# Kernel optimization log

Hardware: AMD Instinct MI355X
Metric: run time of the kernel (lower is better)

The kernel has to match this reference:

```python
import jax, jax.numpy as jnp
import numpy as np

B, N, D, E = 8, 10000, 64, 160000


def setup_inputs() -> dict:
    key = jax.random.key(0)
    ks = jax.random.split(key, 7)
    x = jax.random.normal(ks[0], (B, N, D), dtype=jnp.float32)
    W0 = jax.random.normal(ks[1], (D, D), dtype=jnp.float32) / np.sqrt(D)
    W1 = jax.random.normal(ks[2], (D, D), dtype=jnp.float32) / np.sqrt(D)
    W2 = jax.random.normal(ks[3], (D, D), dtype=jnp.float32) / np.sqrt(D)
    adj_vals = jax.random.uniform(ks[4], (E,), dtype=jnp.float32)
    adj_rows = jax.random.randint(ks[5], (E,), 0, N, dtype=jnp.int32)
    adj_cols = jax.random.randint(ks[6], (E,), 0, N, dtype=jnp.int32)
    return {"x": x, "W0": W0, "W1": W1, "W2": W2,
            "adj_vals": adj_vals, "adj_rows": adj_rows, "adj_cols": adj_cols}


def _spmm(vals, rows, cols, h):
    # h: [B, N, D]; shared sparse adj in COO. out[b, r] += vals[e] * h[b, c]
    msg = h[:, cols, :] * vals[None, :, None]          # [B, E, D]
    return jnp.zeros_like(h).at[:, rows, :].add(msg)   # scatter-add over rows


def _layer(h, W, vals, rows, cols):
    h = jax.nn.relu(jnp.einsum('bnd,df->bnf', h, W))   # Linear (no bias) + act
    return _spmm(vals, rows, cols, h)                  # adj @ h per sample


def reference(x, W0, W1, W2, adj_vals, adj_rows, adj_cols):
    out = _layer(x, W0.T, adj_vals, adj_rows, adj_cols)
    out = _layer(out, W1.T, adj_vals, adj_rows, adj_cols)
    out = _layer(out, W2.T, adj_vals, adj_rows, adj_cols)
    return out
```

## Files before the change

### kernel.cpp

```cpp
#include <hip/hip_runtime.h>
#include <hip/hip_bf16.h>


#define GCN_B 8
#define GCN_N 10000
#define GCN_D 64
#define GCN_E 160000
#define GCN_BN (GCN_B * GCN_N)
#define GCN_CAP 64

typedef __attribute__((ext_vector_type(8))) short short8v;
typedef __attribute__((ext_vector_type(4))) float float4v;

static __device__ __forceinline__ unsigned short f2bf(float f) {
    __hip_bfloat16 h = __float2bfloat16(f);
    return *reinterpret_cast<unsigned short*>(&h);
}

__global__ __launch_bounds__(256) void zero_cvt_kernel(
    int* __restrict__ cur,
    const float* __restrict__ W0, const float* __restrict__ W1,
    const float* __restrict__ W2, unsigned short* __restrict__ Wb)
{
    int i = blockIdx.x * 256 + threadIdx.x;
    if (i < GCN_N) cur[i] = 0;
    if (i < 4096)        Wb[i] = f2bf(W0[i]);
    else if (i < 8192)   Wb[i] = f2bf(W1[i - 4096]);
    else if (i < 12288)  Wb[i] = f2bf(W2[i - 8192]);
}

__global__ __launch_bounds__(256) void scatter_gemm1_kernel(
    const float* __restrict__ vals, const int* __restrict__ rows,
    const int* __restrict__ cols, int* __restrict__ cur,
    float* __restrict__ pval, int* __restrict__ pcol,
    const float* __restrict__ hin,
    const unsigned short* __restrict__ Wb,
    unsigned short* __restrict__ t)
{
    __shared__ unsigned short hs[64 * 72];
    __shared__ unsigned short wsm[64 * 72];

    const int tid = threadIdx.x;

    if (blockIdx.x < 625) {
        int e = blockIdx.x * 256 + tid;
        if (e < GCN_E) {
            int r = rows[e];
            int pos = atomicAdd(&cur[r], 1);
            if (pos < GCN_CAP) {
                pval[(size_t)r * GCN_CAP + pos] = vals[e];
                pcol[(size_t)r * GCN_CAP + pos] = cols[e];
            }
        }
        return;
    }

    const int g0 = (blockIdx.x - 625) * 64;

    {
        const int row = tid >> 2, seg = tid & 3;
        const uint4* src = reinterpret_cast<const uint4*>(Wb + row * 64 + seg * 16);
        uint4 a = src[0], b = src[1];
        *reinterpret_cast<uint4*>(&wsm[row * 72 + seg * 16])     = a;
        *reinterpret_cast<uint4*>(&wsm[row * 72 + seg * 16 + 8]) = b;
    }
    {
        const int row = tid >> 2, seg = tid & 3;
        const int g = g0 + row;
        const int n = g >> 3, b = g & 7;
        const float4* src = reinterpret_cast<const float4*>(
            hin + ((size_t)b * GCN_N + n) * 64 + seg * 16);
        float4 v0 = src[0], v1 = src[1], v2 = src[2], v3 = src[3];
        float vv[16] = {v0.x, v0.y, v0.z, v0.w, v1.x, v1.y, v1.z, v1.w,
                        v2.x, v2.y, v2.z, v2.w, v3.x, v3.y, v3.z, v3.w};
        unsigned int p[8];
#pragma unroll
        for (int j = 0; j < 8; ++j)
            p[j] = (unsigned int)f2bf(vv[2 * j]) |
                   ((unsigned int)f2bf(vv[2 * j + 1]) << 16);
        *reinterpret_cast<uint4*>(&hs[row * 72 + seg * 16]) =
            make_uint4(p[0], p[1], p[2], p[3]);
        *reinterpret_cast<uint4*>(&hs[row * 72 + seg * 16 + 8]) =
            make_uint4(p[4], p[5], p[6], p[7]);
    }
    __syncthreads();

    const int w = tid >> 6;
    const int l = tid & 63;
    const int rbase = w * 16;
    const int arow = rbase + (l & 15);
    const int koff = (l >> 4) * 8;

    float4v acc[4];
#pragma unroll
    for (int nt = 0; nt < 4; ++nt) acc[nt] = (float4v){0.f, 0.f, 0.f, 0.f};

#pragma unroll
    for (int kc = 0; kc < 2; ++kc) {
        short8v afrag = *reinterpret_cast<const short8v*>(
            &hs[arow * 72 + kc * 32 + koff]);
#pragma unroll
        for (int nt = 0; nt < 4; ++nt) {
            short8v bfrag = *reinterpret_cast<const short8v*>(
                &wsm[(nt * 16 + (l & 15)) * 72 + kc * 32 + koff]);
            acc[nt] = __builtin_amdgcn_mfma_f32_16x16x32_bf16(
                afrag, bfrag, acc[nt], 0, 0, 0);
        }
    }

    const int crow = rbase + (l >> 4) * 4;
    const int col = l & 15;
#pragma unroll
    for (int nt = 0; nt < 4; ++nt)
#pragma unroll
        for (int r4 = 0; r4 < 4; ++r4)
            t[(size_t)(g0 + crow + r4) * 64 + nt * 16 + col] =
                f2bf(fmaxf(acc[nt][r4], 0.0f));
}

static __device__ __forceinline__ void gather_row(
    const uint4* __restrict__ t4_in, const float* __restrict__ pval,
    const int* __restrict__ pcol, int r, int deg, int lane, float* a)
{
    const int beg = r * GCN_CAP;
#pragma unroll 8
    for (int j = beg; j < beg + deg; ++j) {
        const float v = pval[j];
        const int c = pcol[j];
        uint4 u = t4_in[(size_t)c * 64 + lane];
        a[0] += v * __uint_as_float(u.x << 16);
        a[1] += v * __uint_as_float(u.x & 0xffff0000u);
        a[2] += v * __uint_as_float(u.y << 16);
        a[3] += v * __uint_as_float(u.y & 0xffff0000u);
        a[4] += v * __uint_as_float(u.z << 16);
        a[5] += v * __uint_as_float(u.z & 0xffff0000u);
        a[6] += v * __uint_as_float(u.w << 16);
        a[7] += v * __uint_as_float(u.w & 0xffff0000u);
    }
}

__global__ __launch_bounds__(512) void spmm_gemm_fused(
    const uint4* __restrict__ t4_in,
    const float* __restrict__ pval,
    const int* __restrict__ pcol,
    const int* __restrict__ deg,
    const unsigned short* __restrict__ Wb,
    unsigned short* __restrict__ t_out)
{
    __shared__ unsigned short hs[64 * 72];
    __shared__ unsigned short wsm[64 * 72];

    const int tid = threadIdx.x;
    const int g0 = blockIdx.x * 64;

    {
        const int row = tid >> 3, seg = tid & 7;
        uint4 v = *reinterpret_cast<const uint4*>(Wb + row * 64 + seg * 8);
        *reinterpret_cast<uint4*>(&wsm[row * 72 + seg * 8]) = v;
    }

    const int w = tid >> 6;
    const int lane = tid & 63;
    const int r = blockIdx.x * 8 + w;
    int d = deg[r]; if (d > GCN_CAP) d = GCN_CAP;

    float a[8];
#pragma unroll
    for (int i = 0; i < 8; ++i) a[i] = 0.f;
    gather_row(t4_in, pval, pcol, r, d, lane, a);

    {
        unsigned int p[4];
#pragma unroll
        for (int k = 0; k < 4; ++k)
            p[k] = (unsigned int)f2bf(a[2 * k]) |
                   ((unsigned int)f2bf(a[2 * k + 1]) << 16);
        *reinterpret_cast<uint4*>(
            &hs[(w * 8 + (lane >> 3)) * 72 + (lane & 7) * 8]) =
            make_uint4(p[0], p[1], p[2], p[3]);
    }
    __syncthreads();

    const int q = w >> 1, pr = w & 1;
    const int arow = q * 16 + (lane & 15);
    const int koff = (lane >> 4) * 8;

    float4v acc[2];
    acc[0] = (float4v){0.f, 0.f, 0.f, 0.f};
    acc[1] = (float4v){0.f, 0.f, 0.f, 0.f};

#pragma unroll
    for (int kc = 0; kc < 2; ++kc) {
        short8v afrag = *reinterpret_cast<const short8v*>(
            &hs[arow * 72 + kc * 32 + koff]);
#pragma unroll
        for (int nt2 = 0; nt2 < 2; ++nt2) {
            const int nt = pr * 2 + nt2;
            short8v bfrag = *reinterpret_cast<const short8v*>(
                &wsm[(nt * 16 + (lane & 15)) * 72 + kc * 32 + koff]);
            acc[nt2] = __builtin_amdgcn_mfma_f32_16x16x32_bf16(
                afrag, bfrag, acc[nt2], 0, 0, 0);
        }
    }

    const int crow = q * 16 + (lane >> 4) * 4;
    const int col = lane & 15;
#pragma unroll
    for (int nt2 = 0; nt2 < 2; ++nt2) {
        const int nt = pr * 2 + nt2;
#pragma unroll
        for (int r4 = 0; r4 < 4; ++r4)
            t_out[(size_t)(g0 + crow + r4) * 64 + nt * 16 + col] =
                f2bf(fmaxf(acc[nt2][r4], 0.0f));
    }
}

__global__ __launch_bounds__(256) void spmm_final(
    const uint4* __restrict__ t4,
    const float* __restrict__ pval,
    const int* __restrict__ pcol,
    const int* __restrict__ deg,
    float* __restrict__ outf)
{
    const int r = (blockIdx.x * 256 + threadIdx.x) >> 6;
    const int lane = threadIdx.x & 63;
    if (r >= GCN_N) return;
    int d = deg[r]; if (d > GCN_CAP) d = GCN_CAP;

    float a[8];
#pragma unroll
    for (int i = 0; i < 8; ++i) a[i] = 0.f;
    gather_row(t4, pval, pcol, r, d, lane, a);

    const int b = lane >> 3;
    const int d0 = (lane & 7) * 8;
    float* op = outf + ((size_t)b * GCN_N + r) * 64 + d0;
    *reinterpret_cast<float4*>(op)     = make_float4(a[0], a[1], a[2], a[3]);
    *reinterpret_cast<float4*>(op + 4) = make_float4(a[4], a[5], a[6], a[7]);
}

extern "C" void kernel_launch(void* const* d_in, const int* in_sizes, int n_in,
                              void* d_out, int out_size, void* d_ws, size_t ws_size,
                              hipStream_t stream) {
    const float* x    = (const float*)d_in[0];
    const float* W0   = (const float*)d_in[1];
    const float* W1   = (const float*)d_in[2];
    const float* W2   = (const float*)d_in[3];
    const float* vals = (const float*)d_in[4];
    const int*   rows = (const int*)d_in[5];
    const int*   cols = (const int*)d_in[6];

    const size_t t_bytes = (size_t)GCN_BN * GCN_D * 2;

    char* ws = (char*)d_ws;
    unsigned short* tA = (unsigned short*)ws;
    size_t off = (t_bytes + 255) / 256 * 256;
    int*   cur  = (int*)(ws + off); off += (GCN_N * 4 + 255) / 256 * 256;
    float* pval = (float*)(ws + off); off += (size_t)GCN_N * GCN_CAP * 4;
    int*   pcol = (int*)(ws + off); off += (size_t)GCN_N * GCN_CAP * 4;
    unsigned short* Wb = (unsigned short*)(ws + off); off += 3 * 4096 * 2;

    unsigned short* t2 = (unsigned short*)d_out;
    float* outf = (float*)d_out;

    const int gemm_grid = GCN_BN / 64;
    const int edge_grid = (GCN_E + 255) / 256;
    const int spmm_grid = (GCN_N * 64 + 255) / 256;

    zero_cvt_kernel<<<48, 256, 0, stream>>>(cur, W0, W1, W2, Wb);
    scatter_gemm1_kernel<<<edge_grid + gemm_grid, 256, 0, stream>>>(
        vals, rows, cols, cur, pval, pcol, x, Wb, tA);

    spmm_gemm_fused<<<gemm_grid, 512, 0, stream>>>(
        (const uint4*)tA, pval, pcol, cur, Wb + 4096, t2);
    spmm_gemm_fused<<<gemm_grid, 512, 0, stream>>>(
        (const uint4*)t2, pval, pcol, cur, Wb + 8192, tA);
    spmm_final<<<spmm_grid, 256, 0, stream>>>((const uint4*)tA, pval, pcol, cur, outf);
}
```

Baseline: 99.59 us.

## Quantize intermediate activations to uint8 with per-row scales for SpMM gathers

Intermediate post-ReLU activations are stored as 8-bit unsigned values with a per-row float scale instead of bf16. The GEMM epilogues compute a row-wise max (via shuffles, or through a shared-memory reduction in the fused kernel) to derive the scale. The gather loops then read half as many bytes per neighbor plus one scale value. This cuts the memory traffic of the random-access gather, at the cost of lower precision, extra syncs and reduction work in the epilogue, and byte-granular stores.

```diff
diff --git a/kernel.cpp b/kernel.cpp
--- a/kernel.cpp
+++ b/kernel.cpp
@@ -35,7 +35,8 @@
     float* __restrict__ pval, int* __restrict__ pcol,
     const float* __restrict__ hin,
     const unsigned short* __restrict__ Wb,
-    unsigned short* __restrict__ t)
+    unsigned char* __restrict__ t8,
+    float* __restrict__ sc)
 {
     __shared__ unsigned short hs[64 * 72];
     __shared__ unsigned short wsm[64 * 72];
@@ -111,41 +112,59 @@
     const int crow = rbase + (l >> 4) * 4;
     const int col = l & 15;
 #pragma unroll
-    for (int nt = 0; nt < 4; ++nt)
-#pragma unroll
-        for (int r4 = 0; r4 < 4; ++r4)
-            t[(size_t)(g0 + crow + r4) * 64 + nt * 16 + col] =
-                f2bf(fmaxf(acc[nt][r4], 0.0f));
-}
-
-static __device__ __forceinline__ void gather_row(
-    const uint4* __restrict__ t4_in, const float* __restrict__ pval,
-    const int* __restrict__ pcol, int r, int deg, int lane, float* a)
+    for (int r4 = 0; r4 < 4; ++r4) {
+        float v0 = fmaxf(acc[0][r4], 0.0f);
+        float v1 = fmaxf(acc[1][r4], 0.0f);
+        float v2 = fmaxf(acc[2][r4], 0.0f);
+        float v3 = fmaxf(acc[3][r4], 0.0f);
+        float m = fmaxf(fmaxf(v0, v1), fmaxf(v2, v3));
+        m = fmaxf(m, __shfl_xor(m, 1, 64));
+        m = fmaxf(m, __shfl_xor(m, 2, 64));
+        m = fmaxf(m, __shfl_xor(m, 4, 64));
+        m = fmaxf(m, __shfl_xor(m, 8, 64));
+        const float inv = (m > 0.0f) ? 255.0f / m : 0.0f;
+        const size_t g = (size_t)(g0 + crow + r4);
+        t8[g * 64 +  0 + col] = (unsigned char)rintf(v0 * inv);
+        t8[g * 64 + 16 + col] = (unsigned char)rintf(v1 * inv);
+        t8[g * 64 + 32 + col] = (unsigned char)rintf(v2 * inv);
+        t8[g * 64 + 48 + col] = (unsigned char)rintf(v3 * inv);
+        if (col == 0) sc[g] = m * (1.0f / 255.0f);
+    }
+}
+
+static __device__ __forceinline__ void gather_row_i8(
+    const uint2* __restrict__ t8, const float* __restrict__ sc,
+    const float* __restrict__ pval, const int* __restrict__ pcol,
+    int r, int deg, int lane, float* a)
 {
     const int beg = r * GCN_CAP;
+    const int bidx = lane >> 3;
 #pragma unroll 8
     for (int j = beg; j < beg + deg; ++j) {
         const float v = pval[j];
         const int c = pcol[j];
-        uint4 u = t4_in[(size_t)c * 64 + lane];
-        a[0] += v * __uint_as_float(u.x << 16);
-        a[1] += v * __uint_as_float(u.x & 0xffff0000u);
-        a[2] += v * __uint_as_float(u.y << 16);
-        a[3] += v * __uint_as_float(u.y & 0xffff0000u);
-        a[4] += v * __uint_as_float(u.z << 16);
-        a[5] += v * __uint_as_float(u.z & 0xffff0000u);
-        a[6] += v * __uint_as_float(u.w << 16);
-        a[7] += v * __uint_as_float(u.w & 0xffff0000u);
+        const float s = v * sc[c * 8 + bidx];
+        uint2 u = t8[(size_t)c * 64 + lane];
+        a[0] += s * (float)( u.x        & 0xff);
+        a[1] += s * (float)((u.x >>  8) & 0xff);
+        a[2] += s * (float)((u.x >> 16) & 0xff);
+        a[3] += s * (float)( u.x >> 24);
+        a[4] += s * (float)( u.y        & 0xff);
+        a[5] += s * (float)((u.y >>  8) & 0xff);
+        a[6] += s * (float)((u.y >> 16) & 0xff);
+        a[7] += s * (float)( u.y >> 24);
     }
 }
 
 __global__ __launch_bounds__(512) void spmm_gemm_fused(
-    const uint4* __restrict__ t4_in,
+    const uint2* __restrict__ t8_in,
+    const float* __restrict__ sc_in,
     const float* __restrict__ pval,
     const int* __restrict__ pcol,
     const int* __restrict__ deg,
     const unsigned short* __restrict__ Wb,
-    unsigned short* __restrict__ t_out)
+    unsigned char* __restrict__ t8_out,
+    float* __restrict__ sc_out)
 {
     __shared__ unsigned short hs[64 * 72];
     __shared__ unsigned short wsm[64 * 72];
@@ -167,7 +186,7 @@
     float a[8];
 #pragma unroll
     for (int i = 0; i < 8; ++i) a[i] = 0.f;
-    gather_row(t4_in, pval, pcol, r, d, lane, a);
+    gather_row_i8(t8_in, sc_in, pval, pcol, r, d, lane, a);
 
     {
         unsigned int p[4];
@@ -205,18 +224,48 @@
 
     const int crow = q * 16 + (lane >> 4) * 4;
     const int col = lane & 15;
-#pragma unroll
-    for (int nt2 = 0; nt2 < 2; ++nt2) {
-        const int nt = pr * 2 + nt2;
+    float v[2][4];
+#pragma unroll
+    for (int nt2 = 0; nt2 < 2; ++nt2)
 #pragma unroll
         for (int r4 = 0; r4 < 4; ++r4)
-            t_out[(size_t)(g0 + crow + r4) * 64 + nt * 16 + col] =
-                f2bf(fmaxf(acc[nt2][r4], 0.0f));
+            v[nt2][r4] = fmaxf(acc[nt2][r4], 0.0f);
+
+    __syncthreads();
+    float* pm = reinterpret_cast<float*>(hs);
+    float* scl = reinterpret_cast<float*>(wsm);
+#pragma unroll
+    for (int r4 = 0; r4 < 4; ++r4)
+        pm[(crow + r4) * 32 + pr * 16 + col] = fmaxf(v[0][r4], v[1][r4]);
+    __syncthreads();
+
+    if (tid < 64) {
+        float m = 0.f;
+        const float* p = &pm[tid * 32];
+#pragma unroll 8
+        for (int j = 0; j < 32; ++j) m = fmaxf(m, p[j]);
+        scl[tid] = m;
+        sc_out[g0 + tid] = m * (1.0f / 255.0f);
+    }
+    __syncthreads();
+
+#pragma unroll
+    for (int r4 = 0; r4 < 4; ++r4) {
+        const float m = scl[crow + r4];
+        const float inv = (m > 0.0f) ? 255.0f / m : 0.0f;
+        const size_t g = (size_t)(g0 + crow + r4);
+#pragma unroll
+        for (int nt2 = 0; nt2 < 2; ++nt2) {
+            const int nt = pr * 2 + nt2;
+            t8_out[g * 64 + nt * 16 + col] =
+                (unsigned char)rintf(v[nt2][r4] * inv);
+        }
     }
 }
 
 __global__ __launch_bounds__(256) void spmm_final(
-    const uint4* __restrict__ t4,
+    const uint2* __restrict__ t8,
+    const float* __restrict__ sc,
     const float* __restrict__ pval,
     const int* __restrict__ pcol,
     const int* __restrict__ deg,
@@ -230,7 +279,7 @@
     float a[8];
 #pragma unroll
     for (int i = 0; i < 8; ++i) a[i] = 0.f;
-    gather_row(t4, pval, pcol, r, d, lane, a);
+    gather_row_i8(t8, sc, pval, pcol, r, d, lane, a);
 
     const int b = lane >> 3;
     const int d0 = (lane & 7) * 8;
@@ -250,17 +299,20 @@
     const int*   rows = (const int*)d_in[5];
     const int*   cols = (const int*)d_in[6];
 
-    const size_t t_bytes = (size_t)GCN_BN * GCN_D * 2;
+    const size_t t8_bytes = (size_t)GCN_BN * GCN_D;
+    const size_t sc_bytes = (size_t)GCN_BN * 4;
 
     char* ws = (char*)d_ws;
-    unsigned short* tA = (unsigned short*)ws;
-    size_t off = (t_bytes + 255) / 256 * 256;
+    unsigned char* tA8 = (unsigned char*)ws;
+    size_t off = (t8_bytes + 255) / 256 * 256;
+    float* scA  = (float*)(ws + off); off += (sc_bytes + 255) / 256 * 256;
+    float* sc2  = (float*)(ws + off); off += (sc_bytes + 255) / 256 * 256;
     int*   cur  = (int*)(ws + off); off += (GCN_N * 4 + 255) / 256 * 256;
     float* pval = (float*)(ws + off); off += (size_t)GCN_N * GCN_CAP * 4;
     int*   pcol = (int*)(ws + off); off += (size_t)GCN_N * GCN_CAP * 4;
     unsigned short* Wb = (unsigned short*)(ws + off); off += 3 * 4096 * 2;
 
-    unsigned short* t2 = (unsigned short*)d_out;
+    unsigned char* t28 = (unsigned char*)d_out;
     float* outf = (float*)d_out;
 
     const int gemm_grid = GCN_BN / 64;
@@ -269,11 +321,12 @@
 
     zero_cvt_kernel<<<48, 256, 0, stream>>>(cur, W0, W1, W2, Wb);
     scatter_gemm1_kernel<<<edge_grid + gemm_grid, 256, 0, stream>>>(
-        vals, rows, cols, cur, pval, pcol, x, Wb, tA);
+        vals, rows, cols, cur, pval, pcol, x, Wb, tA8, scA);
 
     spmm_gemm_fused<<<gemm_grid, 512, 0, stream>>>(
-        (const uint4*)tA, pval, pcol, cur, Wb + 4096, t2);
+        (const uint2*)tA8, scA, pval, pcol, cur, Wb + 4096, t28, sc2);
     spmm_gemm_fused<<<gemm_grid, 512, 0, stream>>>(
-        (const uint4*)t2, pval, pcol, cur, Wb + 8192, tA);
-    spmm_final<<<spmm_grid, 256, 0, stream>>>((const uint4*)tA, pval, pcol, cur, outf);
-}
+        (const uint2*)t28, sc2, pval, pcol, cur, Wb + 8192, tA8, scA);
+    spmm_final<<<spmm_grid, 256, 0, stream>>>(
+        (const uint2*)tA8, scA, pval, pcol, cur, outf);
+}
```

Result: faster. 95.34 us (-4.3%).
